# Kernel tuning notes

Measured on AMD Instinct MI355X. Metric: run time of the kernel, lower is better.

## Reference

```python
import jax, jax.numpy as jnp
import numpy as np

B, H, W, C = 4, 64, 64, 64
DK = C // 8  # key/query channels from Conv2D(filters=channels//8)


def setup_inputs() -> dict:
    key = jax.random.key(0)
    ks = jax.random.split(key, 4)
    x = jax.random.normal(ks[0], (B, H, W, C), dtype=jnp.float32)
    # he_normal-ish scale for 1x1 conv kernels (fan_in = C)
    s = np.sqrt(2.0 / C).astype(np.float32)
    Wf = jax.random.normal(ks[1], (C, DK), dtype=jnp.float32) * s
    Wg = jax.random.normal(ks[2], (C, DK), dtype=jnp.float32) * s
    Wh = jax.random.normal(ks[3], (C, C), dtype=jnp.float32) * s
    bf = jnp.zeros((DK,), dtype=jnp.float32)
    bg = jnp.zeros((DK,), dtype=jnp.float32)
    bh = jnp.zeros((C,), dtype=jnp.float32)
    return {"x": x, "Wf": Wf, "bf": bf, "Wg": Wg, "bg": bg, "Wh": Wh, "bh": bh}


def reference(x, Wf, bf, Wg, bg, Wh, bh):
    b, h, w, c = x.shape
    n = h * w
    xf = x.reshape(b, n, c)  # 1x1 conv == per-position linear over flattened spatial dims
    f = xf @ Wf + bf         # [B, N, DK]
    g = xf @ Wg + bg         # [B, N, DK]
    v = xf @ Wh + bh         # [B, N, C]
    # attention = softmax(g @ f^T) over keys (tf.nn.softmax default: last axis)
    scores = jnp.einsum('bnd,bmd->bnm', g, f)   # [B, N, N]
    attn = jax.nn.softmax(scores, axis=-1)
    out = jnp.einsum('bnm,bmc->bnc', attn, v)   # [B, N, C]
    return out
```

## Files before the change

### kernel.cpp

```cpp
#include <hip/hip_runtime.h>
#include <hip/hip_bf16.h>
#include <hip/hip_fp16.h>

typedef _Float16 half8_t  __attribute__((ext_vector_type(8)));
typedef short    short8_t __attribute__((ext_vector_type(8)));
typedef float    f32x4    __attribute__((ext_vector_type(4)));

#define LOG2E 1.44269504088896f

__global__ __launch_bounds__(256) void prep_kernel(
    const float* __restrict__ x,
    const float* __restrict__ Wf, const float* __restrict__ bf,
    const float* __restrict__ Wg, const float* __restrict__ bg,
    const float* __restrict__ Wh, const float* __restrict__ bh,
    _Float16* __restrict__ fh, _Float16* __restrict__ gh,
    unsigned short* __restrict__ vT)
{
  __shared__ float XsT[64 * 33];
  __shared__ float Wall[64 * 80];
  __shared__ float ball[80];
  const int t  = threadIdx.x;
  const int p0 = blockIdx.x * 32;

  for (int i = t; i < 512; i += 256) {
    Wall[(i >> 3) * 80 + (i & 7)]     = Wf[i];
    Wall[(i >> 3) * 80 + 8 + (i & 7)] = Wg[i] * LOG2E;
  }
  for (int i = t; i < 4096; i += 256)
    Wall[(i >> 6) * 80 + 16 + (i & 63)] = Wh[i];
  if (t < 80) ball[t] = (t < 8) ? bf[t] : (t < 16) ? bg[t - 8] * LOG2E : bh[t - 16];

  const float4* xs = (const float4*)(x + (size_t)p0 * 64);
#pragma unroll
  for (int i = 0; i < 2; i++) {
    int idx = t + i * 256;
    int row = idx >> 4, c4 = idx & 15;
    float4 v = xs[idx];
    XsT[(c4 * 4 + 0) * 33 + row] = v.x;
    XsT[(c4 * 4 + 1) * 33 + row] = v.y;
    XsT[(c4 * 4 + 2) * 33 + row] = v.z;
    XsT[(c4 * 4 + 3) * 33 + row] = v.w;
  }
  __syncthreads();

  const int pos = t & 31;
  const int g   = t >> 5;
  const int cb  = g * 10;

  float acc[10];
#pragma unroll
  for (int j = 0; j < 10; j++) acc[j] = ball[cb + j];

  for (int c = 0; c < 64; c++) {
    float xv = XsT[c * 33 + pos];
    const float2* wr = (const float2*)&Wall[c * 80 + cb];
#pragma unroll
    for (int k = 0; k < 5; k++) {
      float2 w2 = wr[k];
      acc[2 * k]     += xv * w2.x;
      acc[2 * k + 1] += xv * w2.y;
    }
  }

  const size_t pg = (size_t)p0 + pos;
  const int b = (int)(pg >> 12);
  const int n = (int)(pg & 4095);
  const int kblock = n >> 5;
  const int r  = n & 31;
  const int q8 = r >> 3, j8 = r & 7;
  const int slot = (j8 < 4) ? (q8 * 4 + j8) : (16 + q8 * 4 + (j8 - 4));
  const size_t fpos = ((size_t)b * 4096 + (kblock << 5) + slot) * 8;
  const size_t vbase = (((size_t)b * 128 + kblock) << 11) + r;
#pragma unroll
  for (int jj = 0; jj < 10; jj++) {
    int ch = cb + jj;
    if (ch < 8) {
      fh[fpos + ch] = (_Float16)acc[jj];
    } else if (ch < 16) {
      gh[pg * 8 + (ch - 8)] = (_Float16)acc[jj];
    } else {
      __hip_bfloat16 hv = __float2bfloat16(acc[jj]);
      vT[vbase + (size_t)(ch - 16) * 32] = *(unsigned short*)&hv;
    }
  }
}

__device__ __forceinline__ unsigned pack_bf16_2(float lo, float hi) {
  float2 f2; f2.x = lo; f2.y = hi;
  __hip_bfloat162 h2 = __float22bfloat162_rn(f2);
  return *reinterpret_cast<unsigned*>(&h2);
}

__global__ __launch_bounds__(512, 2) void attn_kernel(
    const _Float16* __restrict__ fh,
    const _Float16* __restrict__ gh,
    const unsigned short* __restrict__ vT,
    float* __restrict__ out)
{
  const int N    = 4096;
  const int lane = threadIdx.x & 63;
  const int w    = threadIdx.x >> 6;
  const int quad = lane >> 4;
  const int l15  = lane & 15;

  __shared__ float red[7][64][17];

  const int xcd = blockIdx.x & 7;
  const int b   = xcd >> 1;
  const int qg  = ((blockIdx.x >> 3) << 1) + (xcd & 1);
  const int q0  = qg * 64;
  const int kbase = w * 512;

  const _Float16* fbase = fh + (size_t)b * N * 8;
  const _Float16* gbase = gh + (size_t)b * N * 8;
  const short*    vbat  = (const short*)vT + (size_t)b * 262144 + (l15 << 5) + (quad << 3);

  half8_t gfrag[4] = {{}, {}, {}, {}};
  if (quad == 0) {
#pragma unroll
    for (int tt = 0; tt < 4; tt++)
      gfrag[tt] = *(const half8_t*)(gbase + (size_t)(q0 + tt * 16 + l15) * 8);
  }

  const f32x4 zc = {0.f, 0.f, 0.f, 0.f};
  f32x4 acc[4][4];
  f32x4 acc4[4];
#pragma unroll
  for (int tt = 0; tt < 4; tt++) {
    acc4[tt] = zc;
#pragma unroll
    for (int ct = 0; ct < 4; ct++) acc[tt][ct] = zc;
  }

  short8_t ones8;
#pragma unroll
  for (int i = 0; i < 8; i++) ones8[i] = (short)0x3F80;

  half8_t f0 = {}, f1 = {};

#pragma unroll 2
  for (int cc = 0; cc < 16; cc++) {
    const int k0 = kbase + cc * 32;

    if (quad == 0) {
      f0 = *(const half8_t*)(fbase + (size_t)(k0 + l15) * 8);
      f1 = *(const half8_t*)(fbase + (size_t)(k0 + 16 + l15) * 8);
    }
    const short* vk = vbat + ((size_t)(k0 >> 5) << 11);
    short8_t v0 = *(const short8_t*)(vk);
    short8_t v1 = *(const short8_t*)(vk + 512);
    short8_t v2 = *(const short8_t*)(vk + 1024);
    short8_t v3 = *(const short8_t*)(vk + 1536);

#pragma unroll
    for (int tt = 0; tt < 4; tt++) {
      f32x4 s0 = __builtin_amdgcn_mfma_f32_16x16x32_f16(f0, gfrag[tt], zc, 0, 0, 0);
      f32x4 s1 = __builtin_amdgcn_mfma_f32_16x16x32_f16(f1, gfrag[tt], zc, 0, 0, 0);

      float p00 = __builtin_amdgcn_exp2f(s0[0]), p01 = __builtin_amdgcn_exp2f(s0[1]);
      float p02 = __builtin_amdgcn_exp2f(s0[2]), p03 = __builtin_amdgcn_exp2f(s0[3]);
      float p10 = __builtin_amdgcn_exp2f(s1[0]), p11 = __builtin_amdgcn_exp2f(s1[1]);
      float p12 = __builtin_amdgcn_exp2f(s1[2]), p13 = __builtin_amdgcn_exp2f(s1[3]);

      union { unsigned u[4]; short8_t v; } pu;
      pu.u[0] = pack_bf16_2(p00, p01);
      pu.u[1] = pack_bf16_2(p02, p03);
      pu.u[2] = pack_bf16_2(p10, p11);
      pu.u[3] = pack_bf16_2(p12, p13);
      short8_t pfrag = pu.v;

      acc[tt][0] = __builtin_amdgcn_mfma_f32_16x16x32_bf16(v0, pfrag, acc[tt][0], 0, 0, 0);
      acc[tt][1] = __builtin_amdgcn_mfma_f32_16x16x32_bf16(v1, pfrag, acc[tt][1], 0, 0, 0);
      acc[tt][2] = __builtin_amdgcn_mfma_f32_16x16x32_bf16(v2, pfrag, acc[tt][2], 0, 0, 0);
      acc[tt][3] = __builtin_amdgcn_mfma_f32_16x16x32_bf16(v3, pfrag, acc[tt][3], 0, 0, 0);
      acc4[tt]   = __builtin_amdgcn_mfma_f32_16x16x32_bf16(ones8, pfrag, acc4[tt], 0, 0, 0);
    }
  }

#pragma unroll 1
  for (int tt = 0; tt < 4; tt++) {
    if (w > 0) {
      float* p = &red[w - 1][lane][0];
#pragma unroll
      for (int ct = 0; ct < 4; ct++)
#pragma unroll
        for (int reg = 0; reg < 4; reg++) p[ct * 4 + reg] = acc[tt][ct][reg];
      p[16] = acc4[tt][0];
    }
    __syncthreads();
    if (w == 0) {
      f32x4 a0 = acc[tt][0], a1 = acc[tt][1], a2 = acc[tt][2], a3 = acc[tt][3];
      float lv = acc4[tt][0];
#pragma unroll
      for (int ww = 0; ww < 7; ww++) {
        const float* p = &red[ww][lane][0];
#pragma unroll
        for (int reg = 0; reg < 4; reg++) {
          a0[reg] += p[0 + reg];
          a1[reg] += p[4 + reg];
          a2[reg] += p[8 + reg];
          a3[reg] += p[12 + reg];
        }
        lv += p[16];
      }
      const float inv = 1.0f / lv;
      float* ob = out + ((size_t)b * N + q0 + tt * 16 + l15) * 64 + (quad << 2);
      *(f32x4*)(ob)      = a0 * inv;
      *(f32x4*)(ob + 16) = a1 * inv;
      *(f32x4*)(ob + 32) = a2 * inv;
      *(f32x4*)(ob + 48) = a3 * inv;
    }
    __syncthreads();
  }
}

extern "C" void kernel_launch(void* const* d_in, const int* in_sizes, int n_in,
                              void* d_out, int out_size, void* d_ws, size_t ws_size,
                              hipStream_t stream) {
  const float* x  = (const float*)d_in[0];
  const float* Wf = (const float*)d_in[1];
  const float* bf = (const float*)d_in[2];
  const float* Wg = (const float*)d_in[3];
  const float* bg = (const float*)d_in[4];
  const float* Wh = (const float*)d_in[5];
  const float* bh = (const float*)d_in[6];
  float* out = (float*)d_out;

  char* ws = (char*)d_ws;
  _Float16* fh = (_Float16*)ws;
  _Float16* gh = (_Float16*)(ws + 262144);
  unsigned short* vT = (unsigned short*)(ws + 524288);

  prep_kernel<<<512, 256, 0, stream>>>(x, Wf, bf, Wg, bg, Wh, bh, fh, gh, vT);
  attn_kernel<<<256, 512, 0, stream>>>(fh, gh, vT, out);
}
```

Before: 107.2 us.

## Use MFMA for projection prep and double-buffer K/V loads in attention

```diff
diff --git a/kernel.cpp b/kernel.cpp
--- a/kernel.cpp
+++ b/kernel.cpp
@@ -4,9 +4,16 @@
 
 typedef _Float16 half8_t  __attribute__((ext_vector_type(8)));
 typedef short    short8_t __attribute__((ext_vector_type(8)));
+typedef short    short4_t __attribute__((ext_vector_type(4)));
 typedef float    f32x4    __attribute__((ext_vector_type(4)));
 
 #define LOG2E 1.44269504088896f
+
+__device__ __forceinline__ unsigned pack_bf16_2(float lo, float hi) {
+  float2 f2; f2.x = lo; f2.y = hi;
+  __hip_bfloat162 h2 = __float22bfloat162_rn(f2);
+  return *reinterpret_cast<unsigned*>(&h2);
+}
 
 __global__ __launch_bounds__(256) void prep_kernel(
     const float* __restrict__ x,
@@ -16,79 +23,76 @@
     _Float16* __restrict__ fh, _Float16* __restrict__ gh,
     unsigned short* __restrict__ vT)
 {
-  __shared__ float XsT[64 * 33];
-  __shared__ float Wall[64 * 80];
+  __shared__ _Float16 WtT[80 * 72];
   __shared__ float ball[80];
-  const int t  = threadIdx.x;
-  const int p0 = blockIdx.x * 32;
+  const int t = threadIdx.x;
 
   for (int i = t; i < 512; i += 256) {
-    Wall[(i >> 3) * 80 + (i & 7)]     = Wf[i];
-    Wall[(i >> 3) * 80 + 8 + (i & 7)] = Wg[i] * LOG2E;
-  }
-  for (int i = t; i < 4096; i += 256)
-    Wall[(i >> 6) * 80 + 16 + (i & 63)] = Wh[i];
+    int c = i >> 3, d = i & 7;
+    WtT[d * 72 + c]       = (_Float16)Wf[i];
+    WtT[(8 + d) * 72 + c] = (_Float16)(Wg[i] * LOG2E);
+  }
+  for (int i = t; i < 4096; i += 256) {
+    int c = i >> 6, ch = i & 63;
+    WtT[(16 + ch) * 72 + c] = (_Float16)Wh[i];
+  }
   if (t < 80) ball[t] = (t < 8) ? bf[t] : (t < 16) ? bg[t - 8] * LOG2E : bh[t - 16];
-
-  const float4* xs = (const float4*)(x + (size_t)p0 * 64);
-#pragma unroll
-  for (int i = 0; i < 2; i++) {
-    int idx = t + i * 256;
-    int row = idx >> 4, c4 = idx & 15;
-    float4 v = xs[idx];
-    XsT[(c4 * 4 + 0) * 33 + row] = v.x;
-    XsT[(c4 * 4 + 1) * 33 + row] = v.y;
-    XsT[(c4 * 4 + 2) * 33 + row] = v.z;
-    XsT[(c4 * 4 + 3) * 33 + row] = v.w;
-  }
   __syncthreads();
 
-  const int pos = t & 31;
-  const int g   = t >> 5;
-  const int cb  = g * 10;
-
-  float acc[10];
-#pragma unroll
-  for (int j = 0; j < 10; j++) acc[j] = ball[cb + j];
-
-  for (int c = 0; c < 64; c++) {
-    float xv = XsT[c * 33 + pos];
-    const float2* wr = (const float2*)&Wall[c * 80 + cb];
-#pragma unroll
-    for (int k = 0; k < 5; k++) {
-      float2 w2 = wr[k];
-      acc[2 * k]     += xv * w2.x;
-      acc[2 * k + 1] += xv * w2.y;
-    }
-  }
-
-  const size_t pg = (size_t)p0 + pos;
-  const int b = (int)(pg >> 12);
-  const int n = (int)(pg & 4095);
-  const int kblock = n >> 5;
-  const int r  = n & 31;
-  const int q8 = r >> 3, j8 = r & 7;
-  const int slot = (j8 < 4) ? (q8 * 4 + j8) : (16 + q8 * 4 + (j8 - 4));
-  const size_t fpos = ((size_t)b * 4096 + (kblock << 5) + slot) * 8;
-  const size_t vbase = (((size_t)b * 128 + kblock) << 11) + r;
-#pragma unroll
-  for (int jj = 0; jj < 10; jj++) {
-    int ch = cb + jj;
-    if (ch < 8) {
-      fh[fpos + ch] = (_Float16)acc[jj];
-    } else if (ch < 16) {
-      gh[pg * 8 + (ch - 8)] = (_Float16)acc[jj];
+  const int lane = t & 63, w = t >> 6;
+  const int quad = lane >> 4, l15 = lane & 15;
+  const int p0 = blockIdx.x * 64;
+  const int row = p0 + w * 16 + l15;
+
+  const float* xr = x + (size_t)row * 64 + quad * 8;
+  float4 xa = *(const float4*)(xr);
+  float4 xb = *(const float4*)(xr + 4);
+  float4 xc = *(const float4*)(xr + 32);
+  float4 xd = *(const float4*)(xr + 36);
+  half8_t a0, a1;
+  a0[0]=(_Float16)xa.x; a0[1]=(_Float16)xa.y; a0[2]=(_Float16)xa.z; a0[3]=(_Float16)xa.w;
+  a0[4]=(_Float16)xb.x; a0[5]=(_Float16)xb.y; a0[6]=(_Float16)xb.z; a0[7]=(_Float16)xb.w;
+  a1[0]=(_Float16)xc.x; a1[1]=(_Float16)xc.y; a1[2]=(_Float16)xc.z; a1[3]=(_Float16)xc.w;
+  a1[4]=(_Float16)xd.x; a1[5]=(_Float16)xd.y; a1[6]=(_Float16)xd.z; a1[7]=(_Float16)xd.w;
+
+  const f32x4 zc = {0.f, 0.f, 0.f, 0.f};
+  const int b     = p0 >> 12;
+  const int nbase = (p0 & 4095) + w * 16 + quad * 4;
+  const int kblock = nbase >> 5;
+  const int r0     = nbase & 31;
+  const int q8 = r0 >> 3, j8 = r0 & 7;
+  const int slot0 = (j8 < 4) ? (q8 * 4 + j8) : (16 + q8 * 4 + (j8 - 4));
+  const size_t fbase_out = ((size_t)b * 4096 + (kblock << 5) + slot0) * 8;
+  const size_t gbase_out = ((size_t)p0 + w * 16 + quad * 4) * 8;
+  const size_t vbase_out = (((size_t)b * 128 + kblock) << 11) + r0;
+
+#pragma unroll
+  for (int nt = 0; nt < 5; nt++) {
+    const int ch0 = nt * 16 + l15;
+    const _Float16* wt = &WtT[ch0 * 72 + quad * 8];
+    half8_t b0 = *(const half8_t*)(wt);
+    half8_t b1 = *(const half8_t*)(wt + 32);
+    f32x4 d = __builtin_amdgcn_mfma_f32_16x16x32_f16(a0, b0, zc, 0, 0, 0);
+    d = __builtin_amdgcn_mfma_f32_16x16x32_f16(a1, b1, d, 0, 0, 0);
+    const float bias = ball[ch0];
+    if (nt == 0) {
+      if (l15 < 8) {
+#pragma unroll
+        for (int reg = 0; reg < 4; reg++)
+          fh[fbase_out + (size_t)reg * 8 + l15] = (_Float16)(d[reg] + bias);
+      } else {
+#pragma unroll
+        for (int reg = 0; reg < 4; reg++)
+          gh[gbase_out + (size_t)reg * 8 + (l15 - 8)] = (_Float16)(d[reg] + bias);
+      }
     } else {
-      __hip_bfloat16 hv = __float2bfloat16(acc[jj]);
-      vT[vbase + (size_t)(ch - 16) * 32] = *(unsigned short*)&hv;
-    }
-  }
-}
-
-__device__ __forceinline__ unsigned pack_bf16_2(float lo, float hi) {
-  float2 f2; f2.x = lo; f2.y = hi;
-  __hip_bfloat162 h2 = __float22bfloat162_rn(f2);
-  return *reinterpret_cast<unsigned*>(&h2);
+      const int vch = ch0 - 16;
+      union { unsigned u[2]; short4_t s; } pk;
+      pk.u[0] = pack_bf16_2(d[0] + bias, d[1] + bias);
+      pk.u[1] = pack_bf16_2(d[2] + bias, d[3] + bias);
+      *(short4_t*)(vT + vbase_out + (size_t)vch * 32) = pk.s;
+    }
+  }
 }
 
 __global__ __launch_bounds__(512, 2) void attn_kernel(
@@ -136,45 +140,75 @@
 #pragma unroll
   for (int i = 0; i < 8; i++) ones8[i] = (short)0x3F80;
 
-  half8_t f0 = {}, f1 = {};
-
-#pragma unroll 2
-  for (int cc = 0; cc < 16; cc++) {
-    const int k0 = kbase + cc * 32;
-
+  half8_t  fa0 = {}, fa1 = {}, fb0 = {}, fb1 = {};
+  short8_t va0, va1, va2, va3, vb0, vb1, vb2, vb3;
+
+  {
+    const int k0 = kbase;
     if (quad == 0) {
-      f0 = *(const half8_t*)(fbase + (size_t)(k0 + l15) * 8);
-      f1 = *(const half8_t*)(fbase + (size_t)(k0 + 16 + l15) * 8);
+      fa0 = *(const half8_t*)(fbase + (size_t)(k0 + l15) * 8);
+      fa1 = *(const half8_t*)(fbase + (size_t)(k0 + 16 + l15) * 8);
     }
     const short* vk = vbat + ((size_t)(k0 >> 5) << 11);
-    short8_t v0 = *(const short8_t*)(vk);
-    short8_t v1 = *(const short8_t*)(vk + 512);
-    short8_t v2 = *(const short8_t*)(vk + 1024);
-    short8_t v3 = *(const short8_t*)(vk + 1536);
-
+    va0 = *(const short8_t*)(vk);
+    va1 = *(const short8_t*)(vk + 512);
+    va2 = *(const short8_t*)(vk + 1024);
+    va3 = *(const short8_t*)(vk + 1536);
+  }
+
+  auto compute4 = [&](const half8_t& f0, const half8_t& f1,
+                      const short8_t& v0, const short8_t& v1,
+                      const short8_t& v2, const short8_t& v3) {
 #pragma unroll
     for (int tt = 0; tt < 4; tt++) {
       f32x4 s0 = __builtin_amdgcn_mfma_f32_16x16x32_f16(f0, gfrag[tt], zc, 0, 0, 0);
       f32x4 s1 = __builtin_amdgcn_mfma_f32_16x16x32_f16(f1, gfrag[tt], zc, 0, 0, 0);
-
       float p00 = __builtin_amdgcn_exp2f(s0[0]), p01 = __builtin_amdgcn_exp2f(s0[1]);
       float p02 = __builtin_amdgcn_exp2f(s0[2]), p03 = __builtin_amdgcn_exp2f(s0[3]);
       float p10 = __builtin_amdgcn_exp2f(s1[0]), p11 = __builtin_amdgcn_exp2f(s1[1]);
       float p12 = __builtin_amdgcn_exp2f(s1[2]), p13 = __builtin_amdgcn_exp2f(s1[3]);
-
       union { unsigned u[4]; short8_t v; } pu;
       pu.u[0] = pack_bf16_2(p00, p01);
       pu.u[1] = pack_bf16_2(p02, p03);
       pu.u[2] = pack_bf16_2(p10, p11);
       pu.u[3] = pack_bf16_2(p12, p13);
       short8_t pfrag = pu.v;
-
       acc[tt][0] = __builtin_amdgcn_mfma_f32_16x16x32_bf16(v0, pfrag, acc[tt][0], 0, 0, 0);
       acc[tt][1] = __builtin_amdgcn_mfma_f32_16x16x32_bf16(v1, pfrag, acc[tt][1], 0, 0, 0);
       acc[tt][2] = __builtin_amdgcn_mfma_f32_16x16x32_bf16(v2, pfrag, acc[tt][2], 0, 0, 0);
       acc[tt][3] = __builtin_amdgcn_mfma_f32_16x16x32_bf16(v3, pfrag, acc[tt][3], 0, 0, 0);
       acc4[tt]   = __builtin_amdgcn_mfma_f32_16x16x32_bf16(ones8, pfrag, acc4[tt], 0, 0, 0);
     }
+  };
+
+#pragma unroll 1
+  for (int cc = 0; cc < 16; cc += 2) {
+    {
+      const int k1 = kbase + (cc + 1) * 32;
+      if (quad == 0) {
+        fb0 = *(const half8_t*)(fbase + (size_t)(k1 + l15) * 8);
+        fb1 = *(const half8_t*)(fbase + (size_t)(k1 + 16 + l15) * 8);
+      }
+      const short* vk = vbat + ((size_t)(k1 >> 5) << 11);
+      vb0 = *(const short8_t*)(vk);
+      vb1 = *(const short8_t*)(vk + 512);
+      vb2 = *(const short8_t*)(vk + 1024);
+      vb3 = *(const short8_t*)(vk + 1536);
+    }
+    compute4(fa0, fa1, va0, va1, va2, va3);
+    if (cc + 2 < 16) {
+      const int k2 = kbase + (cc + 2) * 32;
+      if (quad == 0) {
+        fa0 = *(const half8_t*)(fbase + (size_t)(k2 + l15) * 8);
+        fa1 = *(const half8_t*)(fbase + (size_t)(k2 + 16 + l15) * 8);
+      }
+      const short* vk = vbat + ((size_t)(k2 >> 5) << 11);
+      va0 = *(const short8_t*)(vk);
+      va1 = *(const short8_t*)(vk + 512);
+      va2 = *(const short8_t*)(vk + 1024);
+      va3 = *(const short8_t*)(vk + 1536);
+    }
+    compute4(fb0, fb1, vb0, vb1, vb2, vb3);
   }
 
 #pragma unroll 1
@@ -231,6 +265,6 @@
   _Float16* gh = (_Float16*)(ws + 262144);
   unsigned short* vT = (unsigned short*)(ws + 524288);
 
-  prep_kernel<<<512, 256, 0, stream>>>(x, Wf, bf, Wg, bg, Wh, bh, fh, gh, vT);
+  prep_kernel<<<256, 256, 0, stream>>>(x, Wf, bf, Wg, bg, Wh, bh, fh, gh, vT);
   attn_kernel<<<256, 512, 0, stream>>>(fh, gh, vT, out);
 }
```

After: 103.7 us, median of 2. 1.03x faster.
